# Kernel optimization log

Hardware: AMD Instinct MI355X
Metric: run time of the kernel (lower is better)

The kernel has to match this reference:

```python
import jax, jax.numpy as jnp
import numpy as np

KERNEL = 3
DILATIONS = (2, 3)
NUM_HEADS = 8


def _unfold_windows(t, k, dil):
    # t: [B, C, H, W] -> [B, C, k*k, H, W], same layout as nn.Unfold(k, dil, pad=dil*(k-1)//2)
    B, C, H, W = t.shape
    pad = dil * (k - 1) // 2
    tp = jnp.pad(t, ((0, 0), (0, 0), (pad, pad), (pad, pad)))
    ws = [tp[:, :, i * dil:i * dil + H, j * dil:j * dil + W]
          for i in range(k) for j in range(k)]
    return jnp.stack(ws, axis=2)


def _dilate_attention(q, k_, v, kernel, dil, head_dim):
    # q,k_,v: [B, d, H, W]
    B, d, H, W = q.shape
    nh = d // head_dim
    scale = head_dim ** (-0.5)
    qh = q.reshape(B, nh, head_dim, H, W)
    kw = _unfold_windows(k_, kernel, dil).reshape(B, nh, head_dim, kernel * kernel, H, W)
    vw = _unfold_windows(v, kernel, dil).reshape(B, nh, head_dim, kernel * kernel, H, W)
    attn = jax.nn.softmax(jnp.einsum('bndhw,bndkhw->bnkhw', qh, kw) * scale, axis=2)
    out = jnp.einsum('bnkhw,bndkhw->bndhw', attn, vw)  # [B, nh, hd, H, W]
    return out.transpose(0, 3, 4, 1, 2).reshape(B, H, W, d)


def setup_inputs() -> dict:
    key = jax.random.key(0)
    k1, k2, k3, k4 = jax.random.split(key, 4)
    B, H, W, C = 4, 128, 128, 256
    x = jax.random.normal(k1, (B, H, W, C), dtype=jnp.float32)
    Wqkv = jax.random.normal(k2, (3 * C, C), dtype=jnp.float32) * (C ** -0.5)
    Wproj = jax.random.normal(k3, (C, C), dtype=jnp.float32) * (C ** -0.5)
    bproj = jnp.zeros((C,), dtype=jnp.float32)
    return {"x": x, "Wqkv": Wqkv, "Wproj": Wproj, "bproj": bproj}


def reference(x, Wqkv, Wproj, bproj):
    B, H, W, C = x.shape
    nd = len(DILATIONS)
    head_dim = C // NUM_HEADS
    # 1x1 conv qkv (no bias), then split into 3 and nd dilation groups
    qkv = jnp.einsum('bhwc,oc->bohw', x, Wqkv).reshape(B, 3, nd, C // nd, H, W)
    outs = []
    for i, dil in enumerate(DILATIONS):
        q, k_, v = qkv[:, 0, i], qkv[:, 1, i], qkv[:, 2, i]
        outs.append(_dilate_attention(q, k_, v, KERNEL, dil, head_dim))
    xo = jnp.concatenate(outs, axis=-1)  # [B, H, W, C], dilation-group-major channels
    return jnp.einsum('bhwc,oc->bhwo', xo, Wproj) + bproj
```

## Files before the change

### kernel.cpp

```cpp
#include <hip/hip_runtime.h>
#include <stdint.h>


typedef __attribute__((ext_vector_type(8))) short bf16x8;
typedef __attribute__((ext_vector_type(4))) float f32x4;
typedef __attribute__((ext_vector_type(2))) float f32x2;

__device__ __forceinline__ f32x2 up2(unsigned u) {
  union { unsigned u; float f; } a, b;
  a.u = u << 16;
  b.u = u & 0xffff0000u;
  return (f32x2){a.f, b.f};
}
__device__ __forceinline__ unsigned short f2bf(float f) {
  union { float f; unsigned u; } x; x.f = f;
  unsigned r = x.u + 0x7fffu + ((x.u >> 16) & 1u);
  return (unsigned short)(r >> 16);
}
__device__ __forceinline__ unsigned pk2bf(float a, float b) {
  return (unsigned)f2bf(a) | ((unsigned)f2bf(b) << 16);
}

__global__ __launch_bounds__(256) void cvt_f32_to_bf16(
    const float* __restrict__ src, unsigned short* __restrict__ dst, int n) {
  int i = (blockIdx.x * 256 + threadIdx.x) * 8;
  if (i + 8 <= n) {
    const float4* s = (const float4*)(src + i);
    float4 a = s[0], b = s[1];
    uint4 o;
    o.x = pk2bf(a.x, a.y); o.y = pk2bf(a.z, a.w);
    o.z = pk2bf(b.x, b.y); o.w = pk2bf(b.z, b.w);
    *(uint4*)(dst + i) = o;
  } else {
    for (; i < n; ++i) dst[i] = f2bf(src[i]);
  }
}

#define BARX()                                                \
  do {                                                        \
    asm volatile("s_waitcnt lgkmcnt(0)" ::: "memory");        \
    __builtin_amdgcn_s_barrier();                             \
    __builtin_amdgcn_sched_barrier(0);                        \
  } while (0)
#define WAITVM(n)                                             \
  do {                                                        \
    asm volatile("s_waitcnt vmcnt(" #n ")" ::: "memory");     \
    __builtin_amdgcn_sched_barrier(0);                        \
  } while (0)

template <int OUTF32>
__global__ __launch_bounds__(256) void gemm_bt(
    const unsigned short* __restrict__ A, const unsigned short* __restrict__ B,
    void* __restrict__ Cout, const float* __restrict__ bias,
    int N, int NT) {
  __shared__ __align__(16) unsigned short lds[17408];

  const int tid  = threadIdx.x;
  const int lane = tid & 63;
  const int wv   = tid >> 6;
  const int wr   = wv >> 1;
  const int wc   = wv & 1;

  const int nwg = gridDim.x;
  const int q8  = nwg >> 3;
  const int nid = (blockIdx.x & 7) * q8 + (blockIdx.x >> 3);
  const int n0  = (nid % NT) * 128;
  const int m0  = (nid / NT) * 128;

  const int stg_row = wv * 16 + (lane >> 2);
  const int stg_k   = ((lane & 3) ^ ((lane >> 3) & 3)) * 8;
  const unsigned short* Ag = A + (size_t)(m0 + stg_row) * 256 + stg_k;
  const unsigned short* Bg = B + (size_t)(n0 + stg_row) * 256 + stg_k;

  f32x4 acc[4][4];
#pragma unroll
  for (int i = 0; i < 4; ++i)
#pragma unroll
    for (int j = 0; j < 4; ++j) acc[i][j] = (f32x4){0.f, 0.f, 0.f, 0.f};

  const int a_r = lane & 15;

#define STAGE(buf, kt)                                                         \
  do {                                                                         \
    const unsigned short* Asrc = Ag + (kt) * 32;                               \
    const unsigned short* Bsrc = Bg + (kt) * 32;                               \
    _Pragma("unroll")                                                          \
    for (int it = 0; it < 2; ++it) {                                           \
      __builtin_amdgcn_global_load_lds(                                        \
          (const __attribute__((address_space(1))) void*)(Asrc + (size_t)it * 64 * 256), \
          (__attribute__((address_space(3))) void*)&lds[(buf) * 8192 + it * 2048 + wv * 512], \
          16, 0, 0);                                                           \
      __builtin_amdgcn_global_load_lds(                                        \
          (const __attribute__((address_space(1))) void*)(Bsrc + (size_t)it * 64 * 256), \
          (__attribute__((address_space(3))) void*)&lds[(buf) * 8192 + 4096 + it * 2048 + wv * 512], \
          16, 0, 0);                                                           \
    }                                                                          \
  } while (0)

#define COMPUTE(buf)                                                           \
  do {                                                                         \
    const int gsw = (((lane >> 4) ^ ((lane >> 1) & 3))) * 8;                   \
    bf16x8 af[4], bfr[4];                                                      \
    _Pragma("unroll")                                                          \
    for (int mi = 0; mi < 4; ++mi)                                             \
      af[mi] = *(const bf16x8*)&lds[(buf) * 8192 + (wr * 64 + mi * 16 + a_r) * 32 + gsw]; \
    _Pragma("unroll")                                                          \
    for (int ni = 0; ni < 4; ++ni)                                             \
      bfr[ni] = *(const bf16x8*)&lds[(buf) * 8192 + 4096 + (wc * 64 + ni * 16 + a_r) * 32 + gsw]; \
    _Pragma("unroll")                                                          \
    for (int mi = 0; mi < 4; ++mi)                                             \
      _Pragma("unroll")                                                        \
      for (int ni = 0; ni < 4; ++ni)                                           \
        acc[mi][ni] = __builtin_amdgcn_mfma_f32_16x16x32_bf16(                 \
            af[mi], bfr[ni], acc[mi][ni], 0, 0, 0);                            \
  } while (0)

  STAGE(0, 0);
  STAGE(1, 1);
  WAITVM(4);  BARX();
  COMPUTE(0);  BARX();
  STAGE(0, 2); WAITVM(4); BARX();
  COMPUTE(1);  BARX();
  STAGE(1, 3); WAITVM(4); BARX();
  COMPUTE(0);  BARX();
  STAGE(0, 4); WAITVM(4); BARX();
  COMPUTE(1);  BARX();
  STAGE(1, 5); WAITVM(4); BARX();
  COMPUTE(0);  BARX();
  STAGE(0, 6); WAITVM(4); BARX();
  COMPUTE(1);  BARX();
  STAGE(1, 7); WAITVM(4); BARX();
  COMPUTE(0);  BARX();
  WAITVM(0);   BARX();
  COMPUTE(1);  BARX();

  const int cl = wc * 64 + a_r;
  const int rl = wr * 64 + (lane >> 4) * 4;
  if (!OUTF32) {
    unsigned short* eb = &lds[0];
#pragma unroll
    for (int ni = 0; ni < 4; ++ni)
#pragma unroll
      for (int mi = 0; mi < 4; ++mi)
#pragma unroll
        for (int r = 0; r < 4; ++r)
          eb[(rl + mi * 16 + r) * 136 + cl + ni * 16] = f2bf(acc[mi][ni][r]);
    BARX();
    unsigned short* C = (unsigned short*)Cout;
#pragma unroll
    for (int p = 0; p < 8; ++p) {
      const int idx = p * 256 + tid;
      const int row = idx >> 4;
      const int seg = idx & 15;
      uint4 v = *(const uint4*)&eb[row * 136 + seg * 8];
      *(uint4*)&C[(size_t)(m0 + row) * N + n0 + seg * 8] = v;
    }
  } else {
    float* ef = (float*)&lds[0];
    float* C = (float*)Cout;
    float bv[4];
#pragma unroll
    for (int ni = 0; ni < 4; ++ni) bv[ni] = bias[n0 + wc * 64 + ni * 16 + a_r];
#pragma unroll
    for (int half = 0; half < 2; ++half) {
      if (wr == half) {
        const int rb = (lane >> 4) * 4;
#pragma unroll
        for (int ni = 0; ni < 4; ++ni)
#pragma unroll
          for (int mi = 0; mi < 4; ++mi)
#pragma unroll
            for (int r = 0; r < 4; ++r)
              ef[(rb + mi * 16 + r) * 132 + wc * 64 + ni * 16 + a_r] =
                  acc[mi][ni][r] + bv[ni];
      }
      BARX();
#pragma unroll
      for (int p = 0; p < 8; ++p) {
        const int idx = p * 256 + tid;
        const int row = idx >> 5;
        const int seg = idx & 31;
        f32x4 v = *(const f32x4*)&ef[row * 132 + seg * 4];
        *(f32x4*)&C[(size_t)(m0 + half * 64 + row) * N + n0 + seg * 4] = v;
      }
      BARX();
    }
  }
#undef STAGE
#undef COMPUTE
}

__global__ __launch_bounds__(256) void attn_kernel(
    const unsigned short* __restrict__ qkv, unsigned short* __restrict__ xo) {
  __shared__ __align__(16) unsigned short lds[8 * 485 * 8];

  const int nwg = gridDim.x;
  const int q8  = nwg >> 3;
  const int nid = (blockIdx.x & 7) * q8 + (blockIdx.x >> 3);
  const int combo = nid & 7;
  const int tw    = (nid >> 3) & 7;
  const int th    = (nid >> 6) & 7;
  const int b     = nid >> 9;
  const int d     = (combo >> 2) ? 3 : 2;
  const int choff = combo * 32;
  const int h0 = th * 16, w0 = tw * 16;
  const int t = threadIdx.x;

#pragma unroll
  for (int it = 0; it < 16; ++it) {
    const int slot  = it * 256 + t;
    const int px    = slot >> 3;
    const int plane = slot & 7;
    const int r = px / 22, c = px % 22;
    const int gh = h0 - d + r;
    const int gw = w0 - d + c;
    const bool live = (slot < 3872);
    const bool ok = live && ((unsigned)gh < 128u) && ((unsigned)gw < 128u);
    const int hcl = min(max(gh, 0), 127);
    const int wcl = min(max(gw, 0), 127);
    const int gp = (((b << 7) | hcl) << 7) | wcl;
    const unsigned short* src = qkv + (size_t)gp * 768 + 256 +
                                (plane >> 2) * 256 + (plane & 3) * 8 + choff;
    uint4 u = *(const uint4*)src;
    if (!ok) u = make_uint4(0u, 0u, 0u, 0u);
    if (live) *(uint4*)&lds[(plane * 485 + px) * 8] = u;
  }
  __syncthreads();

  const int ph = t >> 4, pw = t & 15;
  const int gp0 = (((b << 7) | (h0 + ph)) << 7) | (w0 + pw);
  const unsigned short* qp = qkv + (size_t)gp0 * 768 + choff;
  f32x2 q2[16];
  {
    uint4 u0 = *(const uint4*)qp;
    uint4 u1 = *(const uint4*)(qp + 8);
    uint4 u2 = *(const uint4*)(qp + 16);
    uint4 u3 = *(const uint4*)(qp + 24);
    const f32x2 s2 = {0.17677669529663687f, 0.17677669529663687f};
    q2[0]  = up2(u0.x) * s2; q2[1]  = up2(u0.y) * s2;
    q2[2]  = up2(u0.z) * s2; q2[3]  = up2(u0.w) * s2;
    q2[4]  = up2(u1.x) * s2; q2[5]  = up2(u1.y) * s2;
    q2[6]  = up2(u1.z) * s2; q2[7]  = up2(u1.w) * s2;
    q2[8]  = up2(u2.x) * s2; q2[9]  = up2(u2.y) * s2;
    q2[10] = up2(u2.z) * s2; q2[11] = up2(u2.w) * s2;
    q2[12] = up2(u3.x) * s2; q2[13] = up2(u3.y) * s2;
    q2[14] = up2(u3.z) * s2; q2[15] = up2(u3.w) * s2;
  }

  float sc[9];
#pragma unroll
  for (int i = 0; i < 3; ++i) {
#pragma unroll
    for (int j = 0; j < 3; ++j) {
      const int lp = (ph + i * d) * 22 + (pw + j * d);
      const uint4 k0 = *(const uint4*)&lds[(0 * 485 + lp) * 8];
      const uint4 k1 = *(const uint4*)&lds[(1 * 485 + lp) * 8];
      const uint4 k2 = *(const uint4*)&lds[(2 * 485 + lp) * 8];
      const uint4 k3 = *(const uint4*)&lds[(3 * 485 + lp) * 8];
      f32x2 p0 = q2[0] * up2(k0.x);
      p0 += q2[1] * up2(k0.y); p0 += q2[2] * up2(k0.z); p0 += q2[3] * up2(k0.w);
      f32x2 p1 = q2[4] * up2(k1.x);
      p1 += q2[5] * up2(k1.y); p1 += q2[6] * up2(k1.z); p1 += q2[7] * up2(k1.w);
      f32x2 p2 = q2[8] * up2(k2.x);
      p2 += q2[9] * up2(k2.y); p2 += q2[10] * up2(k2.z); p2 += q2[11] * up2(k2.w);
      f32x2 p3 = q2[12] * up2(k3.x);
      p3 += q2[13] * up2(k3.y); p3 += q2[14] * up2(k3.z); p3 += q2[15] * up2(k3.w);
      const f32x2 s = (p0 + p1) + (p2 + p3);
      sc[i * 3 + j] = s.x + s.y;
    }
  }

  float mx = sc[0];
#pragma unroll
  for (int k = 1; k < 9; ++k) mx = fmaxf(mx, sc[k]);
  float sum = 0.f;
#pragma unroll
  for (int k = 0; k < 9; ++k) { sc[k] = __expf(sc[k] - mx); sum += sc[k]; }
  const float inv = 1.f / sum;

  f32x2 o2[16];
#pragma unroll
  for (int k = 0; k < 16; ++k) o2[k] = (f32x2){0.f, 0.f};
#pragma unroll
  for (int i = 0; i < 3; ++i) {
#pragma unroll
    for (int j = 0; j < 3; ++j) {
      const int lp = (ph + i * d) * 22 + (pw + j * d);
      const uint4 v0 = *(const uint4*)&lds[(4 * 485 + lp) * 8];
      const uint4 v1 = *(const uint4*)&lds[(5 * 485 + lp) * 8];
      const uint4 v2 = *(const uint4*)&lds[(6 * 485 + lp) * 8];
      const uint4 v3 = *(const uint4*)&lds[(7 * 485 + lp) * 8];
      const float wv = sc[i * 3 + j] * inv;
      const f32x2 w2 = {wv, wv};
      o2[0]  += w2 * up2(v0.x); o2[1]  += w2 * up2(v0.y);
      o2[2]  += w2 * up2(v0.z); o2[3]  += w2 * up2(v0.w);
      o2[4]  += w2 * up2(v1.x); o2[5]  += w2 * up2(v1.y);
      o2[6]  += w2 * up2(v1.z); o2[7]  += w2 * up2(v1.w);
      o2[8]  += w2 * up2(v2.x); o2[9]  += w2 * up2(v2.y);
      o2[10] += w2 * up2(v2.z); o2[11] += w2 * up2(v2.w);
      o2[12] += w2 * up2(v3.x); o2[13] += w2 * up2(v3.y);
      o2[14] += w2 * up2(v3.z); o2[15] += w2 * up2(v3.w);
    }
  }

  unsigned short* op = xo + (size_t)gp0 * 256 + choff;
  uint4 s0, s1, s2o, s3o;
  s0.x  = pk2bf(o2[0].x,  o2[0].y);  s0.y  = pk2bf(o2[1].x,  o2[1].y);
  s0.z  = pk2bf(o2[2].x,  o2[2].y);  s0.w  = pk2bf(o2[3].x,  o2[3].y);
  s1.x  = pk2bf(o2[4].x,  o2[4].y);  s1.y  = pk2bf(o2[5].x,  o2[5].y);
  s1.z  = pk2bf(o2[6].x,  o2[6].y);  s1.w  = pk2bf(o2[7].x,  o2[7].y);
  s2o.x = pk2bf(o2[8].x,  o2[8].y);  s2o.y = pk2bf(o2[9].x,  o2[9].y);
  s2o.z = pk2bf(o2[10].x, o2[10].y); s2o.w = pk2bf(o2[11].x, o2[11].y);
  s3o.x = pk2bf(o2[12].x, o2[12].y); s3o.y = pk2bf(o2[13].x, o2[13].y);
  s3o.z = pk2bf(o2[14].x, o2[14].y); s3o.w = pk2bf(o2[15].x, o2[15].y);
  *(uint4*)op        = s0;
  *(uint4*)(op + 8)  = s1;
  *(uint4*)(op + 16) = s2o;
  *(uint4*)(op + 24) = s3o;
}

extern "C" void kernel_launch(void* const* d_in, const int* in_sizes, int n_in,
                              void* d_out, int out_size, void* d_ws, size_t ws_size,
                              hipStream_t stream) {
  const float* x     = (const float*)d_in[0];
  const float* Wqkv  = (const float*)d_in[1];
  const float* Wproj = (const float*)d_in[2];
  const float* bproj = (const float*)d_in[3];

  const int M = 4 * 128 * 128;
  const int C = 256;

  unsigned short* xb     = (unsigned short*)d_ws;
  unsigned short* qkvb   = xb + (size_t)M * C;
  unsigned short* xob    = qkvb + (size_t)M * 3 * C;
  unsigned short* wqkvb  = xob + (size_t)M * C;
  unsigned short* wprojb = wqkvb + (size_t)3 * C * C;

  cvt_f32_to_bf16<<<(M * C / 8 + 255) / 256, 256, 0, stream>>>(x, xb, M * C);
  cvt_f32_to_bf16<<<(3 * C * C / 8 + 255) / 256, 256, 0, stream>>>(Wqkv, wqkvb, 3 * C * C);
  cvt_f32_to_bf16<<<(C * C / 8 + 255) / 256, 256, 0, stream>>>(Wproj, wprojb, C * C);

  gemm_bt<0><<<(M / 128) * (3 * C / 128), 256, 0, stream>>>(
      xb, wqkvb, (void*)qkvb, nullptr, 3 * C, 3 * C / 128);

  attn_kernel<<<2048, 256, 0, stream>>>(qkvb, xob);

  gemm_bt<1><<<(M / 128) * (C / 128), 256, 0, stream>>>(
      xob, wprojb, d_out, bproj, C, C / 128);
}
```

Baseline: 126.8 us.

## Halve attention LDS by staging K then V, prefetching V into registers

The attention kernel now stages only K in shared memory at first, prefetches V into registers while computing scores and softmax, then overwrites the same LDS region with V. Shared memory per block is halved, which can raise occupancy, and the V global loads overlap with score computation. Q loads are also issued earlier. The cost is two extra barriers and roughly 32 more vector registers held across the score phase, which could limit occupancy.

```diff
diff --git a/kernel.cpp b/kernel.cpp
--- a/kernel.cpp
+++ b/kernel.cpp
@@ -192,7 +192,7 @@
 
 __global__ __launch_bounds__(256) void attn_kernel(
     const unsigned short* __restrict__ qkv, unsigned short* __restrict__ xo) {
-  __shared__ __align__(16) unsigned short lds[8 * 485 * 8];
+  __shared__ __align__(16) unsigned short lds[4 * 485 * 8];
 
   const int nwg = gridDim.x;
   const int q8  = nwg >> 3;
@@ -206,45 +206,58 @@
   const int h0 = th * 16, w0 = tw * 16;
   const int t = threadIdx.x;
 
-#pragma unroll
-  for (int it = 0; it < 16; ++it) {
-    const int slot  = it * 256 + t;
-    const int px    = slot >> 3;
-    const int plane = slot & 7;
+  const int plane = t & 3;
+  const int t4    = t >> 2;
+  const int choffp = choff + plane * 8;
+
+  int  s_gp[8];
+  bool s_ok[8];
+#pragma unroll
+  for (int it = 0; it < 8; ++it) {
+    const int px = it * 64 + t4;
     const int r = px / 22, c = px % 22;
     const int gh = h0 - d + r;
     const int gw = w0 - d + c;
-    const bool live = (slot < 3872);
-    const bool ok = live && ((unsigned)gh < 128u) && ((unsigned)gw < 128u);
+    s_ok[it] = ((unsigned)gh < 128u) && ((unsigned)gw < 128u);
     const int hcl = min(max(gh, 0), 127);
     const int wcl = min(max(gw, 0), 127);
-    const int gp = (((b << 7) | hcl) << 7) | wcl;
-    const unsigned short* src = qkv + (size_t)gp * 768 + 256 +
-                                (plane >> 2) * 256 + (plane & 3) * 8 + choff;
-    uint4 u = *(const uint4*)src;
-    if (!ok) u = make_uint4(0u, 0u, 0u, 0u);
-    if (live) *(uint4*)&lds[(plane * 485 + px) * 8] = u;
-  }
-  __syncthreads();
+    s_gp[it] = (((b << 7) | hcl) << 7) | wcl;
+  }
+
+  const uint4 zz = make_uint4(0u, 0u, 0u, 0u);
 
   const int ph = t >> 4, pw = t & 15;
   const int gp0 = (((b << 7) | (h0 + ph)) << 7) | (w0 + pw);
   const unsigned short* qp = qkv + (size_t)gp0 * 768 + choff;
+  uint4 uq0 = *(const uint4*)qp;
+  uint4 uq1 = *(const uint4*)(qp + 8);
+  uint4 uq2 = *(const uint4*)(qp + 16);
+  uint4 uq3 = *(const uint4*)(qp + 24);
+
+#pragma unroll
+  for (int it = 0; it < 8; ++it) {
+    uint4 u = *(const uint4*)(qkv + (size_t)s_gp[it] * 768 + 256 + choffp);
+    if (!s_ok[it]) u = zz;
+    if (it < 7 || t < 144) *(uint4*)&lds[(plane * 485 + it * 64 + t4) * 8] = u;
+  }
+  __syncthreads();
+
+  uint4 vr[8];
+#pragma unroll
+  for (int it = 0; it < 8; ++it)
+    vr[it] = *(const uint4*)(qkv + (size_t)s_gp[it] * 768 + 512 + choffp);
+
   f32x2 q2[16];
   {
-    uint4 u0 = *(const uint4*)qp;
-    uint4 u1 = *(const uint4*)(qp + 8);
-    uint4 u2 = *(const uint4*)(qp + 16);
-    uint4 u3 = *(const uint4*)(qp + 24);
     const f32x2 s2 = {0.17677669529663687f, 0.17677669529663687f};
-    q2[0]  = up2(u0.x) * s2; q2[1]  = up2(u0.y) * s2;
-    q2[2]  = up2(u0.z) * s2; q2[3]  = up2(u0.w) * s2;
-    q2[4]  = up2(u1.x) * s2; q2[5]  = up2(u1.y) * s2;
-    q2[6]  = up2(u1.z) * s2; q2[7]  = up2(u1.w) * s2;
-    q2[8]  = up2(u2.x) * s2; q2[9]  = up2(u2.y) * s2;
-    q2[10] = up2(u2.z) * s2; q2[11] = up2(u2.w) * s2;
-    q2[12] = up2(u3.x) * s2; q2[13] = up2(u3.y) * s2;
-    q2[14] = up2(u3.z) * s2; q2[15] = up2(u3.w) * s2;
+    q2[0]  = up2(uq0.x) * s2; q2[1]  = up2(uq0.y) * s2;
+    q2[2]  = up2(uq0.z) * s2; q2[3]  = up2(uq0.w) * s2;
+    q2[4]  = up2(uq1.x) * s2; q2[5]  = up2(uq1.y) * s2;
+    q2[6]  = up2(uq1.z) * s2; q2[7]  = up2(uq1.w) * s2;
+    q2[8]  = up2(uq2.x) * s2; q2[9]  = up2(uq2.y) * s2;
+    q2[10] = up2(uq2.z) * s2; q2[11] = up2(uq2.w) * s2;
+    q2[12] = up2(uq3.x) * s2; q2[13] = up2(uq3.y) * s2;
+    q2[14] = up2(uq3.z) * s2; q2[15] = up2(uq3.w) * s2;
   }
 
   float sc[9];
@@ -278,6 +291,15 @@
   for (int k = 0; k < 9; ++k) { sc[k] = __expf(sc[k] - mx); sum += sc[k]; }
   const float inv = 1.f / sum;
 
+  __syncthreads();
+#pragma unroll
+  for (int it = 0; it < 8; ++it) {
+    uint4 u = vr[it];
+    if (!s_ok[it]) u = zz;
+    if (it < 7 || t < 144) *(uint4*)&lds[(plane * 485 + it * 64 + t4) * 8] = u;
+  }
+  __syncthreads();
+
   f32x2 o2[16];
 #pragma unroll
   for (int k = 0; k < 16; ++k) o2[k] = (f32x2){0.f, 0.f};
@@ -286,10 +308,10 @@
 #pragma unroll
     for (int j = 0; j < 3; ++j) {
       const int lp = (ph + i * d) * 22 + (pw + j * d);
-      const uint4 v0 = *(const uint4*)&lds[(4 * 485 + lp) * 8];
-      const uint4 v1 = *(const uint4*)&lds[(5 * 485 + lp) * 8];
-      const uint4 v2 = *(const uint4*)&lds[(6 * 485 + lp) * 8];
-      const uint4 v3 = *(const uint4*)&lds[(7 * 485 + lp) * 8];
+      const uint4 v0 = *(const uint4*)&lds[(0 * 485 + lp) * 8];
+      const uint4 v1 = *(const uint4*)&lds[(1 * 485 + lp) * 8];
+      const uint4 v2 = *(const uint4*)&lds[(2 * 485 + lp) * 8];
+      const uint4 v3 = *(const uint4*)&lds[(3 * 485 + lp) * 8];
       const float wv = sc[i * 3 + j] * inv;
       const f32x2 w2 = {wv, wv};
       o2[0]  += w2 * up2(v0.x); o2[1]  += w2 * up2(v0.y);
```

Measured after the change: 124.0 us. -2.2%, faster.

## Split attention pixels across thread pairs, stage K then V in half-size LDS

Applied to the files above, without the earlier changes.

The attention kernel now uses 512 threads per block, with two threads per pixel each covering half of the 32 head channels. Their partial scores are combined with a lane shuffle. K and V are staged one after the other in a half-size LDS buffer with extra barriers, which cuts LDS and register use per thread to raise occupancy and parallelism. The two weight conversion launches are also merged into one kernel. In exchange, the V load is serialized after the score computation and there are more barriers.

```diff
diff --git a/kernel.cpp b/kernel.cpp
--- a/kernel.cpp
+++ b/kernel.cpp
@@ -34,6 +34,19 @@
   } else {
     for (; i < n; ++i) dst[i] = f2bf(src[i]);
   }
+}
+
+__global__ __launch_bounds__(256) void cvt_w_both(
+    const float* __restrict__ wqkv, const float* __restrict__ wproj,
+    unsigned short* __restrict__ dst) {
+  const int i = (blockIdx.x * 256 + threadIdx.x) * 8;
+  const float* src = (i < 196608) ? (wqkv + i) : (wproj + (i - 196608));
+  const float4* s = (const float4*)src;
+  float4 a = s[0], b = s[1];
+  uint4 o;
+  o.x = pk2bf(a.x, a.y); o.y = pk2bf(a.z, a.w);
+  o.z = pk2bf(b.x, b.y); o.w = pk2bf(b.z, b.w);
+  *(uint4*)(dst + i) = o;
 }
 
 #define BARX()                                                \
@@ -190,9 +203,9 @@
 #undef COMPUTE
 }
 
-__global__ __launch_bounds__(256) void attn_kernel(
+__global__ __launch_bounds__(512) void attn_kernel(
     const unsigned short* __restrict__ qkv, unsigned short* __restrict__ xo) {
-  __shared__ __align__(16) unsigned short lds[8 * 485 * 8];
+  __shared__ __align__(16) unsigned short lds[4 * 485 * 8];
 
   const int nwg = gridDim.x;
   const int q8  = nwg >> 3;
@@ -206,69 +219,59 @@
   const int h0 = th * 16, w0 = tw * 16;
   const int t = threadIdx.x;
 
-#pragma unroll
-  for (int it = 0; it < 16; ++it) {
-    const int slot  = it * 256 + t;
-    const int px    = slot >> 3;
-    const int plane = slot & 7;
+  const int splane = t & 3;
+  const int t4     = t >> 2;
+  const int schoff = choff + splane * 8;
+
+#pragma unroll
+  for (int it = 0; it < 4; ++it) {
+    const int px = it * 128 + t4;
     const int r = px / 22, c = px % 22;
     const int gh = h0 - d + r;
     const int gw = w0 - d + c;
-    const bool live = (slot < 3872);
-    const bool ok = live && ((unsigned)gh < 128u) && ((unsigned)gw < 128u);
+    const bool ok = ((unsigned)gh < 128u) && ((unsigned)gw < 128u);
     const int hcl = min(max(gh, 0), 127);
     const int wcl = min(max(gw, 0), 127);
     const int gp = (((b << 7) | hcl) << 7) | wcl;
-    const unsigned short* src = qkv + (size_t)gp * 768 + 256 +
-                                (plane >> 2) * 256 + (plane & 3) * 8 + choff;
-    uint4 u = *(const uint4*)src;
+    uint4 u = *(const uint4*)(qkv + (size_t)gp * 768 + 256 + schoff);
     if (!ok) u = make_uint4(0u, 0u, 0u, 0u);
-    if (live) *(uint4*)&lds[(plane * 485 + px) * 8] = u;
+    if (it < 3 || t < 400) *(uint4*)&lds[(splane * 485 + px) * 8] = u;
+  }
+
+  const int half = t & 1;
+  const int ph = (t >> 1) >> 4, pw = (t >> 1) & 15;
+  const int gp0 = (((b << 7) | (h0 + ph)) << 7) | (w0 + pw);
+  const unsigned short* qp = qkv + (size_t)gp0 * 768 + choff + half * 16;
+  uint4 uq0 = *(const uint4*)qp;
+  uint4 uq1 = *(const uint4*)(qp + 8);
+  f32x2 q2[8];
+  {
+    const f32x2 s2 = {0.17677669529663687f, 0.17677669529663687f};
+    q2[0] = up2(uq0.x) * s2; q2[1] = up2(uq0.y) * s2;
+    q2[2] = up2(uq0.z) * s2; q2[3] = up2(uq0.w) * s2;
+    q2[4] = up2(uq1.x) * s2; q2[5] = up2(uq1.y) * s2;
+    q2[6] = up2(uq1.z) * s2; q2[7] = up2(uq1.w) * s2;
   }
   __syncthreads();
 
-  const int ph = t >> 4, pw = t & 15;
-  const int gp0 = (((b << 7) | (h0 + ph)) << 7) | (w0 + pw);
-  const unsigned short* qp = qkv + (size_t)gp0 * 768 + choff;
-  f32x2 q2[16];
-  {
-    uint4 u0 = *(const uint4*)qp;
-    uint4 u1 = *(const uint4*)(qp + 8);
-    uint4 u2 = *(const uint4*)(qp + 16);
-    uint4 u3 = *(const uint4*)(qp + 24);
-    const f32x2 s2 = {0.17677669529663687f, 0.17677669529663687f};
-    q2[0]  = up2(u0.x) * s2; q2[1]  = up2(u0.y) * s2;
-    q2[2]  = up2(u0.z) * s2; q2[3]  = up2(u0.w) * s2;
-    q2[4]  = up2(u1.x) * s2; q2[5]  = up2(u1.y) * s2;
-    q2[6]  = up2(u1.z) * s2; q2[7]  = up2(u1.w) * s2;
-    q2[8]  = up2(u2.x) * s2; q2[9]  = up2(u2.y) * s2;
-    q2[10] = up2(u2.z) * s2; q2[11] = up2(u2.w) * s2;
-    q2[12] = up2(u3.x) * s2; q2[13] = up2(u3.y) * s2;
-    q2[14] = up2(u3.z) * s2; q2[15] = up2(u3.w) * s2;
-  }
-
+  const int p0 = 2 * half, p1 = 2 * half + 1;
   float sc[9];
 #pragma unroll
   for (int i = 0; i < 3; ++i) {
 #pragma unroll
     for (int j = 0; j < 3; ++j) {
       const int lp = (ph + i * d) * 22 + (pw + j * d);
-      const uint4 k0 = *(const uint4*)&lds[(0 * 485 + lp) * 8];
-      const uint4 k1 = *(const uint4*)&lds[(1 * 485 + lp) * 8];
-      const uint4 k2 = *(const uint4*)&lds[(2 * 485 + lp) * 8];
-      const uint4 k3 = *(const uint4*)&lds[(3 * 485 + lp) * 8];
-      f32x2 p0 = q2[0] * up2(k0.x);
-      p0 += q2[1] * up2(k0.y); p0 += q2[2] * up2(k0.z); p0 += q2[3] * up2(k0.w);
-      f32x2 p1 = q2[4] * up2(k1.x);
-      p1 += q2[5] * up2(k1.y); p1 += q2[6] * up2(k1.z); p1 += q2[7] * up2(k1.w);
-      f32x2 p2 = q2[8] * up2(k2.x);
-      p2 += q2[9] * up2(k2.y); p2 += q2[10] * up2(k2.z); p2 += q2[11] * up2(k2.w);
-      f32x2 p3 = q2[12] * up2(k3.x);
-      p3 += q2[13] * up2(k3.y); p3 += q2[14] * up2(k3.z); p3 += q2[15] * up2(k3.w);
-      const f32x2 s = (p0 + p1) + (p2 + p3);
-      sc[i * 3 + j] = s.x + s.y;
+      const uint4 k0 = *(const uint4*)&lds[(p0 * 485 + lp) * 8];
+      const uint4 k1 = *(const uint4*)&lds[(p1 * 485 + lp) * 8];
+      f32x2 a = q2[0] * up2(k0.x);
+      a += q2[1] * up2(k0.y); a += q2[2] * up2(k0.z); a += q2[3] * up2(k0.w);
+      a += q2[4] * up2(k1.x); a += q2[5] * up2(k1.y);
+      a += q2[6] * up2(k1.z); a += q2[7] * up2(k1.w);
+      sc[i * 3 + j] = a.x + a.y;
     }
   }
+#pragma unroll
+  for (int k = 0; k < 9; ++k) sc[k] += __shfl_xor(sc[k], 1);
 
   float mx = sc[0];
 #pragma unroll
@@ -278,45 +281,50 @@
   for (int k = 0; k < 9; ++k) { sc[k] = __expf(sc[k] - mx); sum += sc[k]; }
   const float inv = 1.f / sum;
 
-  f32x2 o2[16];
-#pragma unroll
-  for (int k = 0; k < 16; ++k) o2[k] = (f32x2){0.f, 0.f};
+  __syncthreads();
+#pragma unroll
+  for (int it = 0; it < 4; ++it) {
+    const int px = it * 128 + t4;
+    const int r = px / 22, c = px % 22;
+    const int gh = h0 - d + r;
+    const int gw = w0 - d + c;
+    const bool ok = ((unsigned)gh < 128u) && ((unsigned)gw < 128u);
+    const int hcl = min(max(gh, 0), 127);
+    const int wcl = min(max(gw, 0), 127);
+    const int gp = (((b << 7) | hcl) << 7) | wcl;
+    uint4 u = *(const uint4*)(qkv + (size_t)gp * 768 + 512 + schoff);
+    if (!ok) u = make_uint4(0u, 0u, 0u, 0u);
+    if (it < 3 || t < 400) *(uint4*)&lds[(splane * 485 + px) * 8] = u;
+  }
+  __syncthreads();
+
+  f32x2 o2[8];
+#pragma unroll
+  for (int k = 0; k < 8; ++k) o2[k] = (f32x2){0.f, 0.f};
 #pragma unroll
   for (int i = 0; i < 3; ++i) {
 #pragma unroll
     for (int j = 0; j < 3; ++j) {
       const int lp = (ph + i * d) * 22 + (pw + j * d);
-      const uint4 v0 = *(const uint4*)&lds[(4 * 485 + lp) * 8];
-      const uint4 v1 = *(const uint4*)&lds[(5 * 485 + lp) * 8];
-      const uint4 v2 = *(const uint4*)&lds[(6 * 485 + lp) * 8];
-      const uint4 v3 = *(const uint4*)&lds[(7 * 485 + lp) * 8];
+      const uint4 v0 = *(const uint4*)&lds[(p0 * 485 + lp) * 8];
+      const uint4 v1 = *(const uint4*)&lds[(p1 * 485 + lp) * 8];
       const float wv = sc[i * 3 + j] * inv;
       const f32x2 w2 = {wv, wv};
-      o2[0]  += w2 * up2(v0.x); o2[1]  += w2 * up2(v0.y);
-      o2[2]  += w2 * up2(v0.z); o2[3]  += w2 * up2(v0.w);
-      o2[4]  += w2 * up2(v1.x); o2[5]  += w2 * up2(v1.y);
-      o2[6]  += w2 * up2(v1.z); o2[7]  += w2 * up2(v1.w);
-      o2[8]  += w2 * up2(v2.x); o2[9]  += w2 * up2(v2.y);
-      o2[10] += w2 * up2(v2.z); o2[11] += w2 * up2(v2.w);
-      o2[12] += w2 * up2(v3.x); o2[13] += w2 * up2(v3.y);
-      o2[14] += w2 * up2(v3.z); o2[15] += w2 * up2(v3.w);
+      o2[0] += w2 * up2(v0.x); o2[1] += w2 * up2(v0.y);
+      o2[2] += w2 * up2(v0.z); o2[3] += w2 * up2(v0.w);
+      o2[4] += w2 * up2(v1.x); o2[5] += w2 * up2(v1.y);
+      o2[6] += w2 * up2(v1.z); o2[7] += w2 * up2(v1.w);
     }
   }
 
-  unsigned short* op = xo + (size_t)gp0 * 256 + choff;
-  uint4 s0, s1, s2o, s3o;
-  s0.x  = pk2bf(o2[0].x,  o2[0].y);  s0.y  = pk2bf(o2[1].x,  o2[1].y);
-  s0.z  = pk2bf(o2[2].x,  o2[2].y);  s0.w  = pk2bf(o2[3].x,  o2[3].y);
-  s1.x  = pk2bf(o2[4].x,  o2[4].y);  s1.y  = pk2bf(o2[5].x,  o2[5].y);
-  s1.z  = pk2bf(o2[6].x,  o2[6].y);  s1.w  = pk2bf(o2[7].x,  o2[7].y);
-  s2o.x = pk2bf(o2[8].x,  o2[8].y);  s2o.y = pk2bf(o2[9].x,  o2[9].y);
-  s2o.z = pk2bf(o2[10].x, o2[10].y); s2o.w = pk2bf(o2[11].x, o2[11].y);
-  s3o.x = pk2bf(o2[12].x, o2[12].y); s3o.y = pk2bf(o2[13].x, o2[13].y);
-  s3o.z = pk2bf(o2[14].x, o2[14].y); s3o.w = pk2bf(o2[15].x, o2[15].y);
-  *(uint4*)op        = s0;
-  *(uint4*)(op + 8)  = s1;
-  *(uint4*)(op + 16) = s2o;
-  *(uint4*)(op + 24) = s3o;
+  unsigned short* op = xo + (size_t)gp0 * 256 + choff + half * 16;
+  uint4 s0, s1;
+  s0.x = pk2bf(o2[0].x, o2[0].y); s0.y = pk2bf(o2[1].x, o2[1].y);
+  s0.z = pk2bf(o2[2].x, o2[2].y); s0.w = pk2bf(o2[3].x, o2[3].y);
+  s1.x = pk2bf(o2[4].x, o2[4].y); s1.y = pk2bf(o2[5].x, o2[5].y);
+  s1.z = pk2bf(o2[6].x, o2[6].y); s1.w = pk2bf(o2[7].x, o2[7].y);
+  *(uint4*)op       = s0;
+  *(uint4*)(op + 8) = s1;
 }
 
 extern "C" void kernel_launch(void* const* d_in, const int* in_sizes, int n_in,
@@ -337,13 +345,12 @@
   unsigned short* wprojb = wqkvb + (size_t)3 * C * C;
 
   cvt_f32_to_bf16<<<(M * C / 8 + 255) / 256, 256, 0, stream>>>(x, xb, M * C);
-  cvt_f32_to_bf16<<<(3 * C * C / 8 + 255) / 256, 256, 0, stream>>>(Wqkv, wqkvb, 3 * C * C);
-  cvt_f32_to_bf16<<<(C * C / 8 + 255) / 256, 256, 0, stream>>>(Wproj, wprojb, C * C);
+  cvt_w_both<<<128, 256, 0, stream>>>(Wqkv, Wproj, wqkvb);
 
   gemm_bt<0><<<(M / 128) * (3 * C / 128), 256, 0, stream>>>(
       xb, wqkvb, (void*)qkvb, nullptr, 3 * C, 3 * C / 128);
 
-  attn_kernel<<<2048, 256, 0, stream>>>(qkvb, xob);
+  attn_kernel<<<2048, 512, 0, stream>>>(qkvb, xob);
 
   gemm_bt<1><<<(M / 128) * (C / 128), 256, 0, stream>>>(
       xob, wprojb, d_out, bproj, C, C / 128);
```

After: 115.7 us. 1.1x faster.
